# Optimization experiments

Measured on AMD Instinct MI355X. Metric: run time of the kernel, lower is better.

The kernel has to match this reference:

```python
import jax, jax.numpy as jnp
import numpy as np

ALPHA = 0.2
NEG_INF = -1e10


def setup_inputs() -> dict:
    key = jax.random.key(0)
    k1, k2, k3, k4 = jax.random.split(key, 4)
    N, Fin, H, Fout = 4096, 512, 8, 64
    x = jax.random.normal(k1, (N, Fin), dtype=jnp.float32)
    adj = jax.random.randint(k2, (N, N), 0, 2, dtype=jnp.int32)
    W = jax.random.normal(k3, (Fin, H * Fout), dtype=jnp.float32) * (1.0 / np.sqrt(Fin))
    a = jax.random.normal(k4, (2 * Fout, 1), dtype=jnp.float32) * (1.0 / np.sqrt(2 * Fout))
    return {"x": x, "adj": adj, "W": W, "a": a}


def reference(x, adj, W, a):
    N = x.shape[0]
    Fout2 = a.shape[0]          # 2 * out_features
    Fout = Fout2 // 2
    Wh = (x @ W).reshape(N, -1, Fout)          # [N, H, F]
    H = Wh.shape[1]
    # Additive attention decomposes: e[i,j,h] = leakyrelu(a1.Wh[i,h] + a2.Wh[j,h]).
    # This is the exact same math as concatenating [Wh_i; Wh_j] and matmul with a,
    # without materializing the N*N*H*2F tensor.
    a1, a2 = a[:Fout, 0], a[Fout:, 0]
    f1 = jnp.einsum('nhf,f->nh', Wh, a1)       # [N, H]
    f2 = jnp.einsum('nhf,f->nh', Wh, a2)       # [N, H]
    e = jax.nn.leaky_relu(f1[:, None, :] + f2[None, :, :], negative_slope=ALPHA)  # [N, N, H]
    e = jnp.where(adj[:, :, None] > 0, e, NEG_INF)
    attention = jax.nn.softmax(e, axis=1)      # softmax over neighbors j (dim=1)
    # dropout p=0.0 (eval-mode determinism)
    # h_prime[h] = attention[h] @ Wh[h]; then mean over heads
    h_prime = jnp.einsum('ijh,jhf->if', attention, Wh) / H  # [N, F]
    return h_prime
```

## Files before the change

### kernel.cpp

```cpp
#include <hip/hip_runtime.h>

#define LRELU_ALPHA 0.2f

constexpr int NN    = 4096;
constexpr int FIN   = 512;
constexpr int NH    = 8;
constexpr int FOUT  = 64;
constexpr int NFLAT = NH * FOUT;
constexpr float LOG2E = 1.4426950408889634f;

typedef __attribute__((ext_vector_type(8))) __bf16 bf16x8;
typedef __attribute__((ext_vector_type(4))) __bf16 bf16x4;
typedef __attribute__((ext_vector_type(4))) float f32x4;
typedef __attribute__((ext_vector_type(16))) float f32x16;

__device__ __forceinline__ unsigned bitsmear(unsigned mk, int e) {
    return (unsigned)(((int)(mk << (31 - e))) >> 31);
}

__global__ __launch_bounds__(256) void k_prep(const float* __restrict__ W,
                                              __bf16* __restrict__ wtsw) {
    __shared__ float tile[64][68];
    const int bid = blockIdx.x;
    const int t = threadIdx.x;
    const int kt = bid >> 3;
    const int fb = (bid & 7) * 64;
    {
        const int kk = t >> 2, cq = (t & 3) * 16;
        #pragma unroll
        for (int i = 0; i < 4; ++i)
            *(float4*)&tile[kk][cq + i * 4] =
                *(const float4*)&W[(size_t)(kt * 64 + kk) * NFLAT + fb + cq + i * 4];
    }
    __syncthreads();
    const int fl = t >> 2;
    #pragma unroll
    for (int c = 0; c < 2; ++c) {
        int gs = (t & 3) * 2 + c;
        int g  = gs ^ (fl & 7);
        bf16x8 o;
        #pragma unroll
        for (int jo = 0; jo < 8; ++jo) o[jo] = (__bf16)tile[g * 8 + jo][fl];
        *(bf16x8*)&wtsw[((size_t)(kt * NFLAT + fb + fl)) * 64 + gs * 8] = o;
    }
}

__global__ __launch_bounds__(256) void k_main(const float* __restrict__ x,
                                              const int* __restrict__ adj,
                                              const float* __restrict__ av,
                                              const __bf16* __restrict__ wtsw,
                                              __bf16* __restrict__ whtB32,
                                              float* __restrict__ f1T,
                                              float* __restrict__ f2pn,
                                              unsigned long long* __restrict__ bmT) {
    __shared__ alignas(16) __bf16 Bs[2][64 * 64];
    const int bid = blockIdx.x;
    const int t = threadIdx.x;
    if (bid < 512) {
        const int wv = t >> 6, l = t & 63;
        const int jt = bid & 63, h = bid >> 6;
        const int bm = jt * 64, bn = h * 64;
        const int lm = l & 15, lk = l >> 4;
        const int swB = (lm & 7) << 4;

        f32x4 acc[4] = {};
        auto stageB = [&](int kt, int bb) {
            #pragma unroll
            for (int kq = 0; kq < 2; ++kq) {
                int u = t + kq * 256;
                __builtin_amdgcn_global_load_lds(
                    (const __attribute__((address_space(1))) void*)(wtsw + (size_t)(kt * NFLAT + bn) * 64 + u * 8),
                    (__attribute__((address_space(3))) void*)((char*)&Bs[bb][0] + u * 16), 16, 0, 0);
            }
        };

        stageB(0, 0);
        const float* xrow = &x[(size_t)(bm + wv * 16 + lm) * FIN + lk * 8];
        for (int kt = 0; kt < 8; ++kt) {
            bf16x8 aF[2];
            #pragma unroll
            for (int ks = 0; ks < 2; ++ks) {
                float4 u0 = *(const float4*)&xrow[kt * 64 + ks * 32];
                float4 u1 = *(const float4*)&xrow[kt * 64 + ks * 32 + 4];
                bf16x8 af;
                af[0] = (__bf16)u0.x; af[1] = (__bf16)u0.y; af[2] = (__bf16)u0.z; af[3] = (__bf16)u0.w;
                af[4] = (__bf16)u1.x; af[5] = (__bf16)u1.y; af[6] = (__bf16)u1.z; af[7] = (__bf16)u1.w;
                aF[ks] = af;
            }
            __syncthreads();
            if (kt < 7) stageB(kt + 1, (kt + 1) & 1);
            const char* wb = (const char*)&Bs[kt & 1][0];
            #pragma unroll
            for (int q = 0; q < 4; ++q) {
                #pragma unroll
                for (int ks = 0; ks < 2; ++ks) {
                    bf16x8 bF = *(const bf16x8*)(wb + (((q * 16 + lm) * 128 + lk * 16 + ks * 64) ^ swB));
                    acc[q] = __builtin_amdgcn_mfma_f32_16x16x32_bf16(aF[ks], bF, acc[q], 0, 0, 0);
                }
            }
        }
        {
            char* blk = (char*)whtB32 + ((size_t)(h * 64 + jt) << 13);
            const int jg = wv * 2 + (lk >> 1);
            const int j7o = (lk & 1) * 8;
            #pragma unroll
            for (int q = 0; q < 4; ++q) {
                const int f = q * 16 + lm;
                bf16x4 o;
                #pragma unroll
                for (int r = 0; r < 4; ++r) o[r] = (__bf16)acc[q][r];
                *(bf16x4*)(blk + (jg * 64 + f) * 16 + j7o) = o;
            }
        }
        float av1[4], av2[4];
        #pragma unroll
        for (int q = 0; q < 4; ++q) {
            av1[q] = av[q * 16 + lm];
            av2[q] = av[64 + q * 16 + lm];
        }
        float s1[4] = {}, s2[4] = {};
        #pragma unroll
        for (int q = 0; q < 4; ++q)
            #pragma unroll
            for (int r = 0; r < 4; ++r) {
                s1[r] = fmaf(acc[q][r], av1[q], s1[r]);
                s2[r] = fmaf(acc[q][r], av2[q], s2[r]);
            }
        #pragma unroll
        for (int off = 1; off < 16; off <<= 1) {
            #pragma unroll
            for (int r = 0; r < 4; ++r) {
                s1[r] += __shfl_xor(s1[r], off);
                s2[r] += __shfl_xor(s2[r], off);
            }
        }
        if (lm == 0) {
            #pragma unroll
            for (int r = 0; r < 4; ++r) {
                const int io = bm + wv * 16 + lk * 4 + r;
                f1T[h * NN + io] = s1[r] * LOG2E;
                float s2l = s2[r] * LOG2E;
                float2 v = make_float2(exp2f(s2l), exp2f(LRELU_ALPHA * s2l));
                *(float2*)&f2pn[2 * ((size_t)h * NN + io)] = v;
            }
        }
    } else {
        const size_t base = (size_t)(bid - 512) * 16384;
        for (int it = 0; it < 64; ++it) {
            size_t idx = base + (size_t)it * 256 + t;
            int v = adj[idx];
            unsigned long long b = __ballot(v > 0);
            if ((t & 63) == 0) {
                int i = (int)(idx >> 12);
                int jt = (int)((idx >> 6) & 63);
                bmT[(size_t)jt * NN + i] = b;
            }
        }
    }
}

__global__ __launch_bounds__(256, 2) void k_attn(const unsigned long long* __restrict__ bmT,
                                                 const __bf16* __restrict__ whtB32,
                                                 const float* __restrict__ f1T,
                                                 const float* __restrict__ f2pn,
                                                 float* __restrict__ oacc) {
    __shared__ alignas(16) char Ws[4][2][8192];

    const int t   = threadIdx.x;
    const int wv  = t >> 6, l = t & 63;
    const int h   = blockIdx.x & 7;
    const int gi0 = (blockIdx.x >> 3) * 32;
    const int jt0 = wv * 16;

    const int lc = l & 31, hi = l >> 5;
    const int iA = gi0 + lc;
    const float f1v = f1T[h * NN + iA];
    const float E1p = exp2f(f1v);
    const float E1n = exp2f(LRELU_ALPHA * f1v);

    f32x16 acc0 = {}, acc1 = {};
    float lpart = 0.f;

    const char* gsrc = (const char*)whtB32 + ((size_t)(h * 64 + jt0) << 13) + l * 16;
    const char* fptr = (const char*)f2pn + ((size_t)h * NN + (size_t)jt0 * 64) * 8 + hi * 64;
    const unsigned long long* mptr = bmT + (size_t)jt0 * NN + iA;
    char* const wsA = &Ws[wv][0][0];
    char* const wsB = &Ws[wv][1][0];
    const int dsoff = (hi << 10) | (lc << 4);

    auto stage = [&](const char* src, char* dstbase) {
        #pragma unroll
        for (int k = 0; k < 8; ++k)
            __builtin_amdgcn_global_load_lds(
                (const __attribute__((address_space(1))) void*)(src + k * 1024),
                (__attribute__((address_space(3))) void*)(dstbase + l * 16 + k * 1024), 16, 0, 0);
    };
    auto loadF2 = [&](float4* F, const char* fp) {
        #pragma unroll
        for (int js = 0; js < 4; ++js)
            #pragma unroll
            for (int u = 0; u < 4; ++u)
                F[js * 4 + u] = *(const float4*)(fp + js * 128 + u * 16);
    };
    auto compute = [&](const char* wsb, const float4* F, unsigned long long m) {
        const unsigned long long ml = m >> (hi * 8);
        const char* bp = wsb + dsoff;
        #pragma unroll
        for (int js = 0; js < 4; ++js) {
            unsigned mk = (unsigned)(ml >> (16 * js));
            bf16x8 aF;
            #pragma unroll
            for (int u = 0; u < 4; ++u) {
                float4 vv = F[js * 4 + u];
                float a0 = fmaxf(E1p * vv.x, E1n * vv.y);
                float a1 = fmaxf(E1p * vv.z, E1n * vv.w);
                a0 = __uint_as_float(__float_as_uint(a0) & bitsmear(mk, 2 * u));
                a1 = __uint_as_float(__float_as_uint(a1) & bitsmear(mk, 2 * u + 1));
                lpart += a0 + a1;
                aF[2 * u]     = (__bf16)a0;
                aF[2 * u + 1] = (__bf16)a1;
            }
            bf16x8 bF0 = *(const bf16x8*)(bp + js * 2048);
            bf16x8 bF1 = *(const bf16x8*)(bp + js * 2048 + 512);
            __builtin_amdgcn_s_setprio(1);
            acc0 = __builtin_amdgcn_mfma_f32_32x32x16_bf16(aF, bF0, acc0, 0, 0, 0);
            acc1 = __builtin_amdgcn_mfma_f32_32x32x16_bf16(aF, bF1, acc1, 0, 0, 0);
            __builtin_amdgcn_s_setprio(0);
        }
    };

    float4 fA[16], fB[16];
    unsigned long long mA_, mB_;

    stage(gsrc, wsA);
    __builtin_amdgcn_sched_barrier(0);
    loadF2(fA, fptr);
    mA_ = *mptr;
    __builtin_amdgcn_sched_barrier(0);
    gsrc += 8192; fptr += 512; mptr += NN;

    #pragma unroll 1
    for (int jj = 0; jj < 16; jj += 2) {
        stage(gsrc, wsB);
        __builtin_amdgcn_sched_barrier(0);
        loadF2(fB, fptr);
        mB_ = *mptr;
        __builtin_amdgcn_sched_barrier(0);
        gsrc += 8192; fptr += 512; mptr += NN;
        asm volatile("s_waitcnt vmcnt(25)" ::: "memory");
        __builtin_amdgcn_sched_barrier(0);
        compute(wsA, fA, mA_);
        stage(gsrc, wsA);
        __builtin_amdgcn_sched_barrier(0);
        loadF2(fA, fptr);
        mA_ = *mptr;
        __builtin_amdgcn_sched_barrier(0);
        gsrc += 8192; fptr += 512; mptr += NN;
        asm volatile("s_waitcnt vmcnt(25)" ::: "memory");
        __builtin_amdgcn_sched_barrier(0);
        compute(wsB, fB, mB_);
    }

    asm volatile("s_waitcnt vmcnt(0)" ::: "memory");
    __builtin_amdgcn_sched_barrier(0);

    {
        float* Rp = (float*)wsA;
        float* Lp = (float*)wsB;
        #pragma unroll
        for (int reg = 0; reg < 16; ++reg) {
            const int row = (reg & 3) + 8 * (reg >> 2) + 4 * hi;
            Rp[row * 64 + lc]      = acc0[reg];
            Rp[row * 64 + 32 + lc] = acc1[reg];
        }
        Lp[hi * 32 + lc] = lpart;
    }
    __syncthreads();

    {
        const int row = t >> 3, c0 = (t & 7) * 8;
        float ls = 0.f;
        #pragma unroll
        for (int w2 = 0; w2 < 4; ++w2) {
            const float* Lp2 = (const float*)&Ws[w2][1][0];
            ls += Lp2[row] + Lp2[32 + row];
        }
        const float inv = 1.0f / (ls * (float)NH);
        f32x4 s0 = {}, s1 = {};
        #pragma unroll
        for (int w2 = 0; w2 < 4; ++w2) {
            const float* Rp2 = (const float*)&Ws[w2][0][0];
            s0 += *(const f32x4*)&Rp2[row * 64 + c0];
            s1 += *(const f32x4*)&Rp2[row * 64 + c0 + 4];
        }
        float* dst = &oacc[(size_t)(gi0 + row) * NFLAT + h * 64 + c0];
        *(f32x4*)dst       = s0 * inv;
        *(f32x4*)(dst + 4) = s1 * inv;
    }
}

__global__ __launch_bounds__(256) void k_norm(const float* __restrict__ oacc,
                                              float* __restrict__ out) {
    int t = blockIdx.x * 256 + threadIdx.x;
    int i = t >> 4, fq = (t & 15) * 4;
    f32x4 s = {};
    #pragma unroll
    for (int h = 0; h < 8; ++h)
        s += *(const f32x4*)&oacc[(size_t)i * NFLAT + h * 64 + fq];
    *(f32x4*)&out[(size_t)i * FOUT + fq] = s;
}

extern "C" void kernel_launch(void* const* d_in, const int* in_sizes, int n_in,
                              void* d_out, int out_size, void* d_ws, size_t ws_size,
                              hipStream_t stream) {
    const float* x   = (const float*)d_in[0];
    const int*   adj = (const int*)d_in[1];
    const float* W   = (const float*)d_in[2];
    const float* a   = (const float*)d_in[3];
    float* out = (float*)d_out;

    char* ws = (char*)d_ws;
    float* oacc = (float*)ws;           ws += (size_t)NN * NFLAT * 4;
    float* f1T = (float*)ws;            ws += (size_t)NH * NN * 4;
    float* f2pn = (float*)ws;           ws += (size_t)NH * NN * 8;
    __bf16* whtB32 = (__bf16*)ws;       ws += (size_t)NFLAT * NN * 2;
    unsigned long long* bmT = (unsigned long long*)ws; ws += (size_t)NN * NN / 8;
    __bf16* wtsw = (__bf16*)ws;         ws += (size_t)FIN * NFLAT * 2;

    k_prep<<<64, 256, 0, stream>>>(W, wtsw);
    k_main<<<1536, 256, 0, stream>>>(x, adj, a, wtsw, whtB32, f1T, f2pn, bmT);
    k_attn<<<1024, 256, 0, stream>>>(bmT, whtB32, f1T, f2pn, oacc);
    k_norm<<<NN * FOUT / 4 / 256, 256, 0, stream>>>(oacc, out);
}
```

Before: 102.4 us.

## Switch attention path to packed fp16 math and fp16 MFMA

Stores the per-node exponentials f2 as packed fp16 pairs in separate positive/negative arrays and Wh as fp16 instead of bf16. The attention kernel then computes the leaky-relu exponent products, masking and row-sum with packed half2 ops and fdot2, and feeds fp16 MFMA. This cuts VALU work and register and global traffic for the f2 stream, lowering the vmcnt wait. It risks fp16 overflow or underflow, since the exp values and their products can exceed the fp16 range where bf16 or fp32 would not.

```diff
diff --git a/kernel.cpp b/kernel.cpp
--- a/kernel.cpp
+++ b/kernel.cpp
@@ -10,9 +10,12 @@
 constexpr float LOG2E = 1.4426950408889634f;
 
 typedef __attribute__((ext_vector_type(8))) __bf16 bf16x8;
-typedef __attribute__((ext_vector_type(4))) __bf16 bf16x4;
 typedef __attribute__((ext_vector_type(4))) float f32x4;
 typedef __attribute__((ext_vector_type(16))) float f32x16;
+typedef _Float16 f16;
+typedef __attribute__((ext_vector_type(2))) _Float16 f16x2;
+typedef __attribute__((ext_vector_type(4))) _Float16 f16x4;
+typedef __attribute__((ext_vector_type(8))) _Float16 f16x8;
 
 __device__ __forceinline__ unsigned bitsmear(unsigned mk, int e) {
     return (unsigned)(((int)(mk << (31 - e))) >> 31);
@@ -49,9 +52,9 @@
                                               const int* __restrict__ adj,
                                               const float* __restrict__ av,
                                               const __bf16* __restrict__ wtsw,
-                                              __bf16* __restrict__ whtB32,
+                                              f16* __restrict__ whtB16,
                                               float* __restrict__ f1T,
-                                              float* __restrict__ f2pn,
+                                              unsigned* __restrict__ f2pk,
                                               unsigned long long* __restrict__ bmT) {
     __shared__ alignas(16) __bf16 Bs[2][64 * 64];
     const int bid = blockIdx.x;
@@ -100,16 +103,16 @@
             }
         }
         {
-            char* blk = (char*)whtB32 + ((size_t)(h * 64 + jt) << 13);
+            char* blk = (char*)whtB16 + ((size_t)(h * 64 + jt) << 13);
             const int jg = wv * 2 + (lk >> 1);
             const int j7o = (lk & 1) * 8;
             #pragma unroll
             for (int q = 0; q < 4; ++q) {
                 const int f = q * 16 + lm;
-                bf16x4 o;
+                f16x4 o;
                 #pragma unroll
-                for (int r = 0; r < 4; ++r) o[r] = (__bf16)acc[q][r];
-                *(bf16x4*)(blk + (jg * 64 + f) * 16 + j7o) = o;
+                for (int r = 0; r < 4; ++r) o[r] = (f16)acc[q][r];
+                *(f16x4*)(blk + (jg * 64 + f) * 16 + j7o) = o;
             }
         }
         float av1[4], av2[4];
@@ -135,14 +138,22 @@
             }
         }
         if (lm == 0) {
+            float p[4], n[4];
             #pragma unroll
             for (int r = 0; r < 4; ++r) {
                 const int io = bm + wv * 16 + lk * 4 + r;
                 f1T[h * NN + io] = s1[r] * LOG2E;
                 float s2l = s2[r] * LOG2E;
-                float2 v = make_float2(exp2f(s2l), exp2f(LRELU_ALPHA * s2l));
-                *(float2*)&f2pn[2 * ((size_t)h * NN + io)] = v;
-            }
+                p[r] = exp2f(s2l);
+                n[r] = exp2f(LRELU_ALPHA * s2l);
+            }
+            const int io0 = bm + wv * 16 + lk * 4;
+            f16x2 P01 = {(f16)p[0], (f16)p[1]}, P23 = {(f16)p[2], (f16)p[3]};
+            f16x2 N01 = {(f16)n[0], (f16)n[1]}, N23 = {(f16)n[2], (f16)n[3]};
+            uint2 Pv = {__builtin_bit_cast(unsigned, P01), __builtin_bit_cast(unsigned, P23)};
+            uint2 Nv = {__builtin_bit_cast(unsigned, N01), __builtin_bit_cast(unsigned, N23)};
+            *(uint2*)&f2pk[(h * NN + io0) >> 1] = Pv;
+            *(uint2*)&f2pk[(NH * NN / 2) + ((h * NN + io0) >> 1)] = Nv;
         }
     } else {
         const size_t base = (size_t)(bid - 512) * 16384;
@@ -160,9 +171,9 @@
 }
 
 __global__ __launch_bounds__(256, 2) void k_attn(const unsigned long long* __restrict__ bmT,
-                                                 const __bf16* __restrict__ whtB32,
+                                                 const f16* __restrict__ whtB16,
                                                  const float* __restrict__ f1T,
-                                                 const float* __restrict__ f2pn,
+                                                 const unsigned* __restrict__ f2pk,
                                                  float* __restrict__ oacc) {
     __shared__ alignas(16) char Ws[4][2][8192];
 
@@ -175,15 +186,19 @@
     const int lc = l & 31, hi = l >> 5;
     const int iA = gi0 + lc;
     const float f1v = f1T[h * NN + iA];
-    const float E1p = exp2f(f1v);
-    const float E1n = exp2f(LRELU_ALPHA * f1v);
+    const float E1pf = exp2f(f1v);
+    const float E1nf = exp2f(LRELU_ALPHA * f1v);
+    const f16x2 e1p2 = {(f16)E1pf, (f16)E1pf};
+    const f16x2 e1n2 = {(f16)E1nf, (f16)E1nf};
+    const f16x2 one2 = {(f16)1.0f, (f16)1.0f};
 
     f32x16 acc0 = {}, acc1 = {};
     float lpart = 0.f;
 
-    const char* gsrc = (const char*)whtB32 + ((size_t)(h * 64 + jt0) << 13) + l * 16;
-    const char* fptr = (const char*)f2pn + ((size_t)h * NN + (size_t)jt0 * 64) * 8 + hi * 64;
+    const char* gsrc = (const char*)whtB16 + ((size_t)(h * 64 + jt0) << 13) + l * 16;
+    const char* fptr = (const char*)f2pk + (size_t)h * NN * 2 + jt0 * 128 + hi * 16;
     const unsigned long long* mptr = bmT + (size_t)jt0 * NN + iA;
+    constexpr int NOFF = NH * NN * 2;
     char* const wsA = &Ws[wv][0][0];
     char* const wsB = &Ws[wv][1][0];
     const int dsoff = (hi << 10) | (lc << 4);
@@ -195,70 +210,74 @@
                 (const __attribute__((address_space(1))) void*)(src + k * 1024),
                 (__attribute__((address_space(3))) void*)(dstbase + l * 16 + k * 1024), 16, 0, 0);
     };
-    auto loadF2 = [&](float4* F, const char* fp) {
-        #pragma unroll
-        for (int js = 0; js < 4; ++js)
-            #pragma unroll
-            for (int u = 0; u < 4; ++u)
-                F[js * 4 + u] = *(const float4*)(fp + js * 128 + u * 16);
+    auto loadF2 = [&](uint4* FP, uint4* FN, const char* fp) {
+        #pragma unroll
+        for (int js = 0; js < 4; ++js) {
+            FP[js] = *(const uint4*)(fp + js * 32);
+            FN[js] = *(const uint4*)(fp + NOFF + js * 32);
+        }
     };
-    auto compute = [&](const char* wsb, const float4* F, unsigned long long m) {
+    auto compute = [&](const char* wsb, const uint4* FP, const uint4* FN, unsigned long long m) {
         const unsigned long long ml = m >> (hi * 8);
         const char* bp = wsb + dsoff;
         #pragma unroll
         for (int js = 0; js < 4; ++js) {
             unsigned mk = (unsigned)(ml >> (16 * js));
-            bf16x8 aF;
+            const uint4 P4 = FP[js], N4 = FN[js];
+            unsigned r[4];
             #pragma unroll
             for (int u = 0; u < 4; ++u) {
-                float4 vv = F[js * 4 + u];
-                float a0 = fmaxf(E1p * vv.x, E1n * vv.y);
-                float a1 = fmaxf(E1p * vv.z, E1n * vv.w);
-                a0 = __uint_as_float(__float_as_uint(a0) & bitsmear(mk, 2 * u));
-                a1 = __uint_as_float(__float_as_uint(a1) & bitsmear(mk, 2 * u + 1));
-                lpart += a0 + a1;
-                aF[2 * u]     = (__bf16)a0;
-                aF[2 * u + 1] = (__bf16)a1;
-            }
-            bf16x8 bF0 = *(const bf16x8*)(bp + js * 2048);
-            bf16x8 bF1 = *(const bf16x8*)(bp + js * 2048 + 512);
+                unsigned pu = (&P4.x)[u], nu = (&N4.x)[u];
+                f16x2 a = e1p2 * __builtin_bit_cast(f16x2, pu);
+                f16x2 b = e1n2 * __builtin_bit_cast(f16x2, nu);
+                f16x2 mx = __builtin_elementwise_max(a, b);
+                unsigned t0 = bitsmear(mk, 2 * u), t1 = bitsmear(mk, 2 * u + 1);
+                unsigned msk = (t0 & 0x0000FFFFu) | (t1 & 0xFFFF0000u);
+                unsigned rv = __builtin_bit_cast(unsigned, mx) & msk;
+                r[u] = rv;
+                lpart = __builtin_amdgcn_fdot2(__builtin_bit_cast(f16x2, rv), one2, lpart, false);
+            }
+            uint4 ru = {r[0], r[1], r[2], r[3]};
+            f16x8 aF = __builtin_bit_cast(f16x8, ru);
+            f16x8 bF0 = *(const f16x8*)(bp + js * 2048);
+            f16x8 bF1 = *(const f16x8*)(bp + js * 2048 + 512);
             __builtin_amdgcn_s_setprio(1);
-            acc0 = __builtin_amdgcn_mfma_f32_32x32x16_bf16(aF, bF0, acc0, 0, 0, 0);
-            acc1 = __builtin_amdgcn_mfma_f32_32x32x16_bf16(aF, bF1, acc1, 0, 0, 0);
+            acc0 = __builtin_amdgcn_mfma_f32_32x32x16_f16(aF, bF0, acc0, 0, 0, 0);
+            acc1 = __builtin_amdgcn_mfma_f32_32x32x16_f16(aF, bF1, acc1, 0, 0, 0);
             __builtin_amdgcn_s_setprio(0);
         }
     };
 
-    float4 fA[16], fB[16];
+    uint4 fAP[4], fAN[4], fBP[4], fBN[4];
     unsigned long long mA_, mB_;
 
     stage(gsrc, wsA);
     __builtin_amdgcn_sched_barrier(0);
-    loadF2(fA, fptr);
+    loadF2(fAP, fAN, fptr);
     mA_ = *mptr;
     __builtin_amdgcn_sched_barrier(0);
-    gsrc += 8192; fptr += 512; mptr += NN;
+    gsrc += 8192; fptr += 128; mptr += NN;
 
     #pragma unroll 1
     for (int jj = 0; jj < 16; jj += 2) {
         stage(gsrc, wsB);
         __builtin_amdgcn_sched_barrier(0);
-        loadF2(fB, fptr);
+        loadF2(fBP, fBN, fptr);
         mB_ = *mptr;
         __builtin_amdgcn_sched_barrier(0);
-        gsrc += 8192; fptr += 512; mptr += NN;
-        asm volatile("s_waitcnt vmcnt(25)" ::: "memory");
-        __builtin_amdgcn_sched_barrier(0);
-        compute(wsA, fA, mA_);
+        gsrc += 8192; fptr += 128; mptr += NN;
+        asm volatile("s_waitcnt vmcnt(17)" ::: "memory");
+        __builtin_amdgcn_sched_barrier(0);
+        compute(wsA, fAP, fAN, mA_);
         stage(gsrc, wsA);
         __builtin_amdgcn_sched_barrier(0);
-        loadF2(fA, fptr);
+        loadF2(fAP, fAN, fptr);
         mA_ = *mptr;
         __builtin_amdgcn_sched_barrier(0);
-        gsrc += 8192; fptr += 512; mptr += NN;
-        asm volatile("s_waitcnt vmcnt(25)" ::: "memory");
-        __builtin_amdgcn_sched_barrier(0);
-        compute(wsB, fB, mB_);
+        gsrc += 8192; fptr += 128; mptr += NN;
+        asm volatile("s_waitcnt vmcnt(17)" ::: "memory");
+        __builtin_amdgcn_sched_barrier(0);
+        compute(wsB, fBP, fBN, mB_);
     }
 
     asm volatile("s_waitcnt vmcnt(0)" ::: "memory");
@@ -322,13 +341,13 @@
     char* ws = (char*)d_ws;
     float* oacc = (float*)ws;           ws += (size_t)NN * NFLAT * 4;
     float* f1T = (float*)ws;            ws += (size_t)NH * NN * 4;
-    float* f2pn = (float*)ws;           ws += (size_t)NH * NN * 8;
-    __bf16* whtB32 = (__bf16*)ws;       ws += (size_t)NFLAT * NN * 2;
+    unsigned* f2pk = (unsigned*)ws;     ws += (size_t)192 * 1024;
+    f16* whtB16 = (f16*)ws;             ws += (size_t)NFLAT * NN * 2;
     unsigned long long* bmT = (unsigned long long*)ws; ws += (size_t)NN * NN / 8;
     __bf16* wtsw = (__bf16*)ws;         ws += (size_t)FIN * NFLAT * 2;
 
     k_prep<<<64, 256, 0, stream>>>(W, wtsw);
-    k_main<<<1536, 256, 0, stream>>>(x, adj, a, wtsw, whtB32, f1T, f2pn, bmT);
-    k_attn<<<1024, 256, 0, stream>>>(bmT, whtB32, f1T, f2pn, oacc);
+    k_main<<<1536, 256, 0, stream>>>(x, adj, a, wtsw, whtB16, f1T, f2pk, bmT);
+    k_attn<<<1024, 256, 0, stream>>>(bmT, whtB16, f1T, f2pk, oacc);
     k_norm<<<NN * FOUT / 4 / 256, 256, 0, stream>>>(oacc, out);
 }
```

After: 89.40 us. -12.7%, faster.
